# Performance work log

Measured on AMD Instinct MI355X. Metric: run time of the kernel, lower is better.

Reference implementation:

```python
import jax, jax.numpy as jnp
import numpy as np

B, T, E, H, V, O = 64, 512, 128, 256, 100000, 1


def setup_inputs() -> dict:
    key = jax.random.key(0)
    ks = jax.random.split(key, 10)
    sE, sH = 1.0 / np.sqrt(E), 1.0 / np.sqrt(H)
    return {
        "x": jax.random.randint(ks[0], (B, T), 0, V),
        "emb_table": jax.random.normal(ks[1], (V, E), jnp.float32) * 0.1,
        "W_ih": jax.random.normal(ks[2], (4 * H, E), jnp.float32) * sE,  # torch gate order i,f,g,o
        "W_hh": jax.random.normal(ks[3], (4 * H, H), jnp.float32) * sH,
        "b_ih": jnp.zeros((4 * H,), jnp.float32),  # biases init'd to 0 in source
        "b_hh": jnp.zeros((4 * H,), jnp.float32),
        "Wm": jax.random.normal(ks[4], (H, H), jnp.float32) * sH,
        "bm": jnp.zeros((H,), jnp.float32),
        "Wf": jax.random.normal(ks[5], (O, H), jnp.float32) * sH,
        "bf": jnp.zeros((O,), jnp.float32),
    }


def reference(x, emb_table, W_ih, W_hh, b_ih, b_hh, Wm, bm, Wf, bf):
    batch = x.shape[0]
    hid = W_hh.shape[1]
    # vectorized replacement for the per-(i,j) python-loop embedding copy
    embeds = emb_table[x]                                  # [B,T,E]
    # precompute input contribution to all gates for every timestep
    gx = jnp.einsum('bte,ge->btg', embeds, W_ih) + b_ih     # [B,T,4H]
    gx = jnp.swapaxes(gx, 0, 1)                             # [T,B,4H]
    h0 = jnp.zeros((batch, hid), embeds.dtype)
    c0 = jnp.zeros((batch, hid), embeds.dtype)

    def step(carry, g_t):
        h, c = carry
        g = g_t + h @ W_hh.T + b_hh                         # [B,4H]
        i, f, gg, o = jnp.split(g, 4, axis=-1)
        i, f, o = jax.nn.sigmoid(i), jax.nn.sigmoid(f), jax.nn.sigmoid(o)
        c = f * c + i * jnp.tanh(gg)
        h = o * jnp.tanh(c)
        return (h, c), h

    (hT, cT), hs = jax.lax.scan(step, (h0, c0), gx)
    out = jnp.swapaxes(hs, 0, 1)                            # [B,T,H]
    out = out @ Wm.T + bm                                   # ffmiddle
    out = out @ Wf.T + bf                                   # fc -> [B,T,O]
    sig_out = jax.nn.sigmoid(out).reshape(batch, -1).mean(axis=1)  # [B]
    # hidden = (h_n, c_n) with leading num_layers=1 dim, as in torch
    return sig_out, hT[None, :, :], cT[None, :, :]
```

## Files before the change

### kernel.cpp

```cpp
#include <hip/hip_runtime.h>


#define BATCH 64
#define TSTEPS 512
#define EDIM 128
#define HDIM 256
#define G4H 1024

typedef short bf16x8 __attribute__((ext_vector_type(8)));
typedef short bf16x4 __attribute__((ext_vector_type(4)));
typedef float f32x4 __attribute__((ext_vector_type(4)));

__device__ __forceinline__ unsigned short f2bf(float f) {
  unsigned u = __builtin_bit_cast(unsigned, f);
  return (unsigned short)((u + 0x7fffu + ((u >> 16) & 1u)) >> 16);
}
__device__ __forceinline__ float bf2f(unsigned short h) {
  unsigned u = ((unsigned)h) << 16;
  return __builtin_bit_cast(float, u);
}
__device__ __forceinline__ unsigned pk2(float a, float b) {
  return (unsigned)f2bf(a) | ((unsigned)f2bf(b) << 16);
}
__device__ __forceinline__ float fsig(float x) {
  return __builtin_amdgcn_rcpf(1.f + __expf(-x));
}
__device__ __forceinline__ float ftanh(float x) {
  return 1.f - 2.f * __builtin_amdgcn_rcpf(__expf(2.f * x) + 1.f);
}
__device__ __forceinline__ bf16x8 ldfrag(const unsigned short* p) {
  bf16x4 a = *(const bf16x4*)p;
  bf16x4 b = *(const bf16x4*)(p + 16);
  return __builtin_shufflevector(a, b, 0, 1, 2, 3, 4, 5, 6, 7);
}

__global__ __launch_bounds__(256) void k_gx(const int* __restrict__ x,
                                            const float* __restrict__ emb,
                                            const float* __restrict__ Wih,
                                            const float* __restrict__ bih,
                                            unsigned short* __restrict__ gx3) {
  const int t = blockIdx.x;
  const int g0 = blockIdx.y * 64;
  const int tid = threadIdx.x;
  __shared__ unsigned short Al[64 * 136];
  __shared__ unsigned short Bl[64 * 136];
  __shared__ int tok[64];
  if (tid < 64) tok[tid] = x[tid * TSTEPS + t];
  __syncthreads();
  {
    const int r = tid >> 2, c0 = (tid & 3) * 32;
    const float* asrc = emb + (size_t)tok[r] * EDIM + c0;
    const float* bsrc = Wih + (size_t)(g0 + r) * EDIM + c0;
#pragma unroll
    for (int s = 0; s < 32; s += 8) {
      float4 a0 = *(const float4*)(asrc + s);
      float4 a1 = *(const float4*)(asrc + s + 4);
      uint4 pa = {pk2(a0.x, a0.y), pk2(a0.z, a0.w), pk2(a1.x, a1.y), pk2(a1.z, a1.w)};
      *(uint4*)&Al[r * 136 + c0 + s] = pa;
      float4 b0 = *(const float4*)(bsrc + s);
      float4 b1 = *(const float4*)(bsrc + s + 4);
      uint4 pb = {pk2(b0.x, b0.y), pk2(b0.z, b0.w), pk2(b1.x, b1.y), pk2(b1.z, b1.w)};
      *(uint4*)&Bl[r * 136 + c0 + s] = pb;
    }
  }
  __syncthreads();
  const int lane = tid & 63, w = tid >> 6;
  const int lo = lane & 15, hi = lane >> 4;
  const int mb = (w & 1) * 32, nb = (w >> 1) * 32;
  f32x4 acc[2][2];
#pragma unroll
  for (int jj = 0; jj < 2; ++jj) {
    float bv = bih[g0 + nb + jj * 16 + lo];
    acc[0][jj] = (f32x4){bv, bv, bv, bv};
    acc[1][jj] = acc[0][jj];
  }
#pragma unroll
  for (int kk = 0; kk < 4; ++kk) {
    bf16x8 af0 = ldfrag(&Al[(mb + lo) * 136 + kk * 32 + hi * 4]);
    bf16x8 af1 = ldfrag(&Al[(mb + 16 + lo) * 136 + kk * 32 + hi * 4]);
    bf16x8 bf0 = ldfrag(&Bl[(nb + lo) * 136 + kk * 32 + hi * 4]);
    bf16x8 bf1 = ldfrag(&Bl[(nb + 16 + lo) * 136 + kk * 32 + hi * 4]);
    acc[0][0] = __builtin_amdgcn_mfma_f32_16x16x32_bf16(af0, bf0, acc[0][0], 0, 0, 0);
    acc[0][1] = __builtin_amdgcn_mfma_f32_16x16x32_bf16(af0, bf1, acc[0][1], 0, 0, 0);
    acc[1][0] = __builtin_amdgcn_mfma_f32_16x16x32_bf16(af1, bf0, acc[1][0], 0, 0, 0);
    acc[1][1] = __builtin_amdgcn_mfma_f32_16x16x32_bf16(af1, bf1, acc[1][1], 0, 0, 0);
  }
#pragma unroll
  for (int i = 0; i < 2; ++i)
#pragma unroll
    for (int jj = 0; jj < 2; ++jj)
#pragma unroll
      for (int r = 0; r < 4; ++r) {
        int m = mb + i * 16 + hi * 4 + r;
        int col = g0 + nb + jj * 16 + lo;
        int grp = m >> 4, mm = m & 15;
        int bhi = mm >> 2, br = mm & 3;
        int g = col >> 8, jc = col & 255;
        int halfb = jc >> 7, wv = (jc >> 4) & 7, lov = jc & 15;
        size_t idx = (((size_t)(t * 8 + grp * 2 + halfb) * 8 + wv) * 64 +
                      (bhi * 16 + lov)) * 16 + (g * 4 + br);
        gx3[idx] = f2bf(acc[i][jj][r]);
      }
}

__global__ __launch_bounds__(512) void k_rec(const unsigned short* __restrict__ gx3,
                                             const float* __restrict__ Whh,
                                             const float* __restrict__ bhh,
                                             unsigned long long* __restrict__ hx,
                                             unsigned short* __restrict__ hs,
                                             float* __restrict__ out) {
  const int tid = threadIdx.x;
  const int bp = blockIdx.x;
  const int grp = bp >> 1, half = bp & 1;
  const int b0 = grp * 16;
  const int lane = tid & 63, w = tid >> 6;
  const int lo = lane & 15, hi = lane >> 4;
  const int j = half * 128 + w * 16 + lo;
  __shared__ unsigned short h_lds[2][32 * 136];
  bf16x8 wf[4][8];
  float bhv[4];
#pragma unroll
  for (int g = 0; g < 4; ++g) {
    const float* wr = Whh + (size_t)(g * 256 + j) * HDIM;
    bhv[g] = bhh[g * 256 + j];
#pragma unroll
    for (int kk = 0; kk < 8; ++kk) {
      const float* p = wr + kk * 32 + hi * 8;
      float4 v0 = *(const float4*)p;
      float4 v1 = *(const float4*)(p + 4);
      bf16x8 f;
      f[0] = (short)f2bf(v0.x); f[1] = (short)f2bf(v0.y);
      f[2] = (short)f2bf(v0.z); f[3] = (short)f2bf(v0.w);
      f[4] = (short)f2bf(v1.x); f[5] = (short)f2bf(v1.y);
      f[6] = (short)f2bf(v1.z); f[7] = (short)f2bf(v1.w);
      wf[g][kk] = f;
    }
  }
  for (int i = tid; i < 32 * 136 / 2; i += 512) ((unsigned*)h_lds[0])[i] = 0u;
  const unsigned short* gp = gx3 + (((size_t)bp * 8 + w) * 64 + lane) * 16;
  unsigned gw[8];
  {
    uint4 a = *(const uint4*)(gp);
    uint4 b = *(const uint4*)(gp + 8);
    gw[0] = a.x; gw[1] = a.y; gw[2] = a.z; gw[3] = a.w;
    gw[4] = b.x; gw[5] = b.y; gw[6] = b.z; gw[7] = b.w;
  }
  float c[4] = {0.f, 0.f, 0.f, 0.f};
  const int ob = (j >> 3) * 136 + (j & 7);
  const int jp = ((half ^ 1) * 128) + ((tid >> 6) << 4) + (tid & 15);
  const int hip = (tid >> 4) & 3;
  const int pb = (jp >> 3) * 136 + (jp & 7);
  __syncthreads();
  for (int t = 0; t < TSTEPS; ++t) {
    const int cur = t & 1, nxt = cur ^ 1;
    uint4 gA, gB;
    if (t < TSTEPS - 1) {
      const unsigned short* q = gp + (size_t)(t + 1) * 65536;
      gA = *(const uint4*)(q);
      gB = *(const uint4*)(q + 8);
    }
    f32x4 acc[4];
#pragma unroll
    for (int g = 0; g < 4; ++g)
#pragma unroll
      for (int r = 0; r < 4; ++r) {
        unsigned word = gw[g * 2 + (r >> 1)];
        unsigned short v = (r & 1) ? (unsigned short)(word >> 16) : (unsigned short)word;
        acc[g][r] = bf2f(v) + bhv[g];
      }
#pragma unroll
    for (int kk = 0; kk < 8; ++kk) {
      bf16x8 a = *(const bf16x8*)&h_lds[cur][(kk * 4 + hi) * 136 + lo * 8];
      acc[0] = __builtin_amdgcn_mfma_f32_16x16x32_bf16(a, wf[0][kk], acc[0], 0, 0, 0);
      acc[1] = __builtin_amdgcn_mfma_f32_16x16x32_bf16(a, wf[1][kk], acc[1], 0, 0, 0);
      acc[2] = __builtin_amdgcn_mfma_f32_16x16x32_bf16(a, wf[2][kk], acc[2], 0, 0, 0);
      acc[3] = __builtin_amdgcn_mfma_f32_16x16x32_bf16(a, wf[3][kk], acc[3], 0, 0, 0);
    }
    gw[0] = gA.x; gw[1] = gA.y; gw[2] = gA.z; gw[3] = gA.w;
    gw[4] = gB.x; gw[5] = gB.y; gw[6] = gB.z; gw[7] = gB.w;
    float hv[4];
    unsigned short hbf[4];
#pragma unroll
    for (int r = 0; r < 4; ++r) {
      float iv = fsig(acc[0][r]);
      float fv = fsig(acc[1][r]);
      float gv = ftanh(acc[2][r]);
      float ov = fsig(acc[3][r]);
      c[r] = fv * c[r] + iv * gv;
      hv[r] = ov * ftanh(c[r]);
      hbf[r] = f2bf(hv[r]);
    }
    if (t == TSTEPS - 1) {
#pragma unroll
      for (int r = 0; r < 4; ++r) {
        const int b = b0 + hi * 4 + r;
        hs[((size_t)t * BATCH + b) * HDIM + j] = hbf[r];
        out[64 + b * HDIM + j] = hv[r];
        out[64 + BATCH * HDIM + b * HDIM + j] = c[r];
      }
      break;
    }
    const int par = (t + 1) & 1;
    const unsigned wt = (unsigned)(t + 1);
    {
      const unsigned long long tg = ((unsigned long long)wt) << 32;
      unsigned long long* dst = &hx[((size_t)(par * 8 + bp)) * 1024 + w * 128 + lane * 2];
      __hip_atomic_store(&dst[0], tg | (unsigned long long)pk2(hv[0], hv[1]),
                         __ATOMIC_RELAXED, __HIP_MEMORY_SCOPE_AGENT);
      __hip_atomic_store(&dst[1], tg | (unsigned long long)pk2(hv[2], hv[3]),
                         __ATOMIC_RELAXED, __HIP_MEMORY_SCOPE_AGENT);
    }
#pragma unroll
    for (int r = 0; r < 4; ++r) h_lds[nxt][ob + (hi * 4 + r) * 8] = hbf[r];
    {
      unsigned long long v0, v1;
      unsigned long long* src = &hx[((size_t)(par * 8 + (bp ^ 1))) * 1024 + tid * 2];
      do {
        v0 = __hip_atomic_load(&src[0], __ATOMIC_RELAXED, __HIP_MEMORY_SCOPE_AGENT);
        v1 = __hip_atomic_load(&src[1], __ATOMIC_RELAXED, __HIP_MEMORY_SCOPE_AGENT);
      } while ((unsigned)(v0 >> 32) != wt || (unsigned)(v1 >> 32) != wt);
      h_lds[nxt][pb + (hip * 4 + 0) * 8] = (unsigned short)v0;
      h_lds[nxt][pb + (hip * 4 + 1) * 8] = (unsigned short)(v0 >> 16);
      h_lds[nxt][pb + (hip * 4 + 2) * 8] = (unsigned short)v1;
      h_lds[nxt][pb + (hip * 4 + 3) * 8] = (unsigned short)(v1 >> 16);
    }
#pragma unroll
    for (int r = 0; r < 4; ++r)
      hs[((size_t)t * BATCH + (b0 + hi * 4 + r)) * HDIM + j] = hbf[r];
    __syncthreads();
  }
}

__global__ __launch_bounds__(256) void k_weff(const float* __restrict__ Wm,
                                              const float* __restrict__ bm,
                                              const float* __restrict__ Wf,
                                              const float* __restrict__ bfb,
                                              float* __restrict__ weff) {
  const int k = threadIdx.x;
  __shared__ float red[256];
  float acc = 0.f;
#pragma unroll 8
  for (int jj = 0; jj < 256; ++jj) acc += Wf[jj] * Wm[jj * 256 + k];
  weff[k] = acc;
  red[k] = bm[k] * Wf[k];
  __syncthreads();
  for (int s = 128; s > 0; s >>= 1) {
    if (k < s) red[k] += red[k + s];
    __syncthreads();
  }
  if (k == 0) weff[256] = red[0] + bfb[0];
}

__global__ __launch_bounds__(256) void k_sig(const unsigned short* __restrict__ hs,
                                             const float* __restrict__ weff,
                                             float* __restrict__ out) {
  const int b = blockIdx.x;
  const int tid = threadIdx.x, lane = tid & 63, w = tid >> 6;
  __shared__ float wlds[4];
  const float4 w4 = *(const float4*)&weff[lane * 4];
  const float c0 = weff[256];
  float acc = 0.f;
  for (int row = w; row < TSTEPS; row += 4) {
    const unsigned short* hp = &hs[((size_t)row * BATCH + b) * HDIM + lane * 4];
    ushort4 h4 = *(const ushort4*)hp;
    float s = bf2f(h4.x) * w4.x + bf2f(h4.y) * w4.y +
              bf2f(h4.z) * w4.z + bf2f(h4.w) * w4.w;
    s += __shfl_xor(s, 1);  s += __shfl_xor(s, 2);  s += __shfl_xor(s, 4);
    s += __shfl_xor(s, 8);  s += __shfl_xor(s, 16); s += __shfl_xor(s, 32);
    acc += fsig(s + c0);
  }
  if (lane == 0) wlds[w] = acc;
  __syncthreads();
  if (tid == 0) out[b] = (wlds[0] + wlds[1] + wlds[2] + wlds[3]) * (1.f / 512.f);
}

extern "C" void kernel_launch(void* const* d_in, const int* in_sizes, int n_in,
                              void* d_out, int out_size, void* d_ws, size_t ws_size,
                              hipStream_t stream) {
  (void)in_sizes; (void)n_in; (void)out_size; (void)ws_size;
  const int* x = (const int*)d_in[0];
  const float* emb = (const float*)d_in[1];
  const float* Wih = (const float*)d_in[2];
  const float* Whh = (const float*)d_in[3];
  const float* bih = (const float*)d_in[4];
  const float* bhh = (const float*)d_in[5];
  const float* Wm  = (const float*)d_in[6];
  const float* bm  = (const float*)d_in[7];
  const float* Wf  = (const float*)d_in[8];
  const float* bf  = (const float*)d_in[9];
  float* out = (float*)d_out;
  char* ws = (char*)d_ws;
  const size_t gx_bytes = (size_t)TSTEPS * BATCH * G4H * 2;
  const size_t hs_bytes = (size_t)TSTEPS * BATCH * HDIM * 2;
  const size_t hx_bytes = (size_t)2 * 8 * 1024 * 8;
  unsigned short* gx3 = (unsigned short*)ws;
  unsigned short* hs = (unsigned short*)(ws + gx_bytes);
  unsigned long long* hx = (unsigned long long*)(ws + gx_bytes + hs_bytes);
  float* weff = (float*)(ws + gx_bytes + hs_bytes + hx_bytes);
  hipMemsetAsync(hx, 0, hx_bytes, stream);
  k_gx<<<dim3(512, 16), 256, 0, stream>>>(x, emb, Wih, bih, gx3);
  k_weff<<<1, 256, 0, stream>>>(Wm, bm, Wf, bf, weff);
  k_rec<<<8, 512, 0, stream>>>(gx3, Whh, bhh, hx, hs, out);
  k_sig<<<64, 256, 0, stream>>>(hs, weff, out);
}
```

Measured before the change: 1.249 ms.

## Process two batch groups per recurrence block and fuse output head into recurrence

The recurrence kernel now runs on 4 blocks instead of 8, each handling two 16-row batch groups. The two independent MFMA chains are interleaved, so each step's latency-bound chain and cross-block handshake are amortized over twice the work. The sigmoid/mean head is computed inside the recurrence from LDS after each step, which removes the hs buffer and the separate k_sig launch. The gx store is also packed into 64-bit writes. The cost is double the per-step serial work per block (more MFMAs, activations and polls) and higher register pressure, which may lengthen the critical path.

```diff
diff --git a/kernel.cpp b/kernel.cpp
--- a/kernel.cpp
+++ b/kernel.cpp
@@ -88,35 +88,34 @@
 #pragma unroll
   for (int i = 0; i < 2; ++i)
 #pragma unroll
-    for (int jj = 0; jj < 2; ++jj)
-#pragma unroll
-      for (int r = 0; r < 4; ++r) {
-        int m = mb + i * 16 + hi * 4 + r;
-        int col = g0 + nb + jj * 16 + lo;
-        int grp = m >> 4, mm = m & 15;
-        int bhi = mm >> 2, br = mm & 3;
-        int g = col >> 8, jc = col & 255;
-        int halfb = jc >> 7, wv = (jc >> 4) & 7, lov = jc & 15;
-        size_t idx = (((size_t)(t * 8 + grp * 2 + halfb) * 8 + wv) * 64 +
-                      (bhi * 16 + lov)) * 16 + (g * 4 + br);
-        gx3[idx] = f2bf(acc[i][jj][r]);
-      }
-}
-
-__global__ __launch_bounds__(512) void k_rec(const unsigned short* __restrict__ gx3,
-                                             const float* __restrict__ Whh,
-                                             const float* __restrict__ bhh,
-                                             unsigned long long* __restrict__ hx,
-                                             unsigned short* __restrict__ hs,
-                                             float* __restrict__ out) {
+    for (int jj = 0; jj < 2; ++jj) {
+      int grp = (w & 1) * 2 + i;
+      int col = g0 + nb + jj * 16 + lo;
+      int g = col >> 8, jc = col & 255;
+      int halfb = jc >> 7, wv = (jc >> 4) & 7, lov = jc & 15;
+      size_t base = (((size_t)(t * 8 + grp * 2 + halfb) * 8 + wv) * 64 +
+                     (hi * 16 + lov)) * 16 + g * 4;
+      unsigned long long val =
+          (unsigned long long)pk2(acc[i][jj][0], acc[i][jj][1]) |
+          ((unsigned long long)pk2(acc[i][jj][2], acc[i][jj][3]) << 32);
+      *(unsigned long long*)&gx3[base] = val;
+    }
+}
+
+__global__ __launch_bounds__(512, 2) void k_rec(const unsigned short* __restrict__ gx3,
+                                                const float* __restrict__ Whh,
+                                                const float* __restrict__ bhh,
+                                                const float* __restrict__ weff,
+                                                unsigned long long* __restrict__ hx,
+                                                float* __restrict__ out) {
   const int tid = threadIdx.x;
   const int bp = blockIdx.x;
-  const int grp = bp >> 1, half = bp & 1;
-  const int b0 = grp * 16;
+  const int gpair = bp >> 1, half = bp & 1;
+  const int gA = gpair * 2, gB = gpair * 2 + 1;
   const int lane = tid & 63, w = tid >> 6;
   const int lo = lane & 15, hi = lane >> 4;
   const int j = half * 128 + w * 16 + lo;
-  __shared__ unsigned short h_lds[2][32 * 136];
+  __shared__ unsigned short h_lds[2][2][32 * 136];
   bf16x8 wf[4][8];
   float bhv[4];
 #pragma unroll
@@ -136,98 +135,170 @@
       wf[g][kk] = f;
     }
   }
-  for (int i = tid; i < 32 * 136 / 2; i += 512) ((unsigned*)h_lds[0])[i] = 0u;
-  const unsigned short* gp = gx3 + (((size_t)bp * 8 + w) * 64 + lane) * 16;
-  unsigned gw[8];
+  float wv8[8];
   {
-    uint4 a = *(const uint4*)(gp);
-    uint4 b = *(const uint4*)(gp + 8);
-    gw[0] = a.x; gw[1] = a.y; gw[2] = a.z; gw[3] = a.w;
-    gw[4] = b.x; gw[5] = b.y; gw[6] = b.z; gw[7] = b.w;
-  }
-  float c[4] = {0.f, 0.f, 0.f, 0.f};
+    const float* wp = weff + (lane & 31) * 8;
+#pragma unroll
+    for (int e = 0; e < 8; ++e) wv8[e] = wp[e];
+  }
+  const float c0 = weff[256];
+  for (int i = tid; i < 2 * 32 * 136 / 2; i += 512) {
+    ((unsigned*)h_lds[0][0])[i & (32 * 136 / 2 - 1)] = 0u;
+    ((unsigned*)h_lds[1][0])[i & (32 * 136 / 2 - 1)] = 0u;
+  }
+  const unsigned short* gpA = gx3 + (((size_t)(gA * 2 + half) * 8 + w) * 64 + lane) * 16;
+  const unsigned short* gpB = gx3 + (((size_t)(gB * 2 + half) * 8 + w) * 64 + lane) * 16;
+  unsigned gwA[8], gwB[8];
+  {
+    uint4 a = *(const uint4*)(gpA);
+    uint4 b = *(const uint4*)(gpA + 8);
+    gwA[0] = a.x; gwA[1] = a.y; gwA[2] = a.z; gwA[3] = a.w;
+    gwA[4] = b.x; gwA[5] = b.y; gwA[6] = b.z; gwA[7] = b.w;
+    uint4 c = *(const uint4*)(gpB);
+    uint4 d = *(const uint4*)(gpB + 8);
+    gwB[0] = c.x; gwB[1] = c.y; gwB[2] = c.z; gwB[3] = c.w;
+    gwB[4] = d.x; gwB[5] = d.y; gwB[6] = d.z; gwB[7] = d.w;
+  }
+  float cA[4] = {0.f, 0.f, 0.f, 0.f}, cB[4] = {0.f, 0.f, 0.f, 0.f};
+  float hvA[4], hvB[4];
+  float sig_acc = 0.f;
   const int ob = (j >> 3) * 136 + (j & 7);
   const int jp = ((half ^ 1) * 128) + ((tid >> 6) << 4) + (tid & 15);
   const int hip = (tid >> 4) & 3;
   const int pb = (jp >> 3) * 136 + (jp & 7);
+  const int sA = gA * 2 + half, sB = gB * 2 + half;
   __syncthreads();
   for (int t = 0; t < TSTEPS; ++t) {
     const int cur = t & 1, nxt = cur ^ 1;
-    uint4 gA, gB;
+    uint4 pA0, pA1, pB0, pB1;
     if (t < TSTEPS - 1) {
-      const unsigned short* q = gp + (size_t)(t + 1) * 65536;
-      gA = *(const uint4*)(q);
-      gB = *(const uint4*)(q + 8);
-    }
-    f32x4 acc[4];
+      const unsigned short* qA = gpA + (size_t)(t + 1) * 65536;
+      const unsigned short* qB = gpB + (size_t)(t + 1) * 65536;
+      pA0 = *(const uint4*)(qA);
+      pA1 = *(const uint4*)(qA + 8);
+      pB0 = *(const uint4*)(qB);
+      pB1 = *(const uint4*)(qB + 8);
+    }
+    f32x4 accA[4], accB[4];
 #pragma unroll
     for (int g = 0; g < 4; ++g)
 #pragma unroll
       for (int r = 0; r < 4; ++r) {
-        unsigned word = gw[g * 2 + (r >> 1)];
-        unsigned short v = (r & 1) ? (unsigned short)(word >> 16) : (unsigned short)word;
-        acc[g][r] = bf2f(v) + bhv[g];
+        unsigned wa = gwA[g * 2 + (r >> 1)];
+        unsigned wb = gwB[g * 2 + (r >> 1)];
+        unsigned short va = (r & 1) ? (unsigned short)(wa >> 16) : (unsigned short)wa;
+        unsigned short vb = (r & 1) ? (unsigned short)(wb >> 16) : (unsigned short)wb;
+        accA[g][r] = bf2f(va) + bhv[g];
+        accB[g][r] = bf2f(vb) + bhv[g];
       }
 #pragma unroll
     for (int kk = 0; kk < 8; ++kk) {
-      bf16x8 a = *(const bf16x8*)&h_lds[cur][(kk * 4 + hi) * 136 + lo * 8];
-      acc[0] = __builtin_amdgcn_mfma_f32_16x16x32_bf16(a, wf[0][kk], acc[0], 0, 0, 0);
-      acc[1] = __builtin_amdgcn_mfma_f32_16x16x32_bf16(a, wf[1][kk], acc[1], 0, 0, 0);
-      acc[2] = __builtin_amdgcn_mfma_f32_16x16x32_bf16(a, wf[2][kk], acc[2], 0, 0, 0);
-      acc[3] = __builtin_amdgcn_mfma_f32_16x16x32_bf16(a, wf[3][kk], acc[3], 0, 0, 0);
-    }
-    gw[0] = gA.x; gw[1] = gA.y; gw[2] = gA.z; gw[3] = gA.w;
-    gw[4] = gB.x; gw[5] = gB.y; gw[6] = gB.z; gw[7] = gB.w;
-    float hv[4];
-    unsigned short hbf[4];
+      bf16x8 a = *(const bf16x8*)&h_lds[0][cur][(kk * 4 + hi) * 136 + lo * 8];
+      accA[0] = __builtin_amdgcn_mfma_f32_16x16x32_bf16(a, wf[0][kk], accA[0], 0, 0, 0);
+      accA[1] = __builtin_amdgcn_mfma_f32_16x16x32_bf16(a, wf[1][kk], accA[1], 0, 0, 0);
+      accA[2] = __builtin_amdgcn_mfma_f32_16x16x32_bf16(a, wf[2][kk], accA[2], 0, 0, 0);
+      accA[3] = __builtin_amdgcn_mfma_f32_16x16x32_bf16(a, wf[3][kk], accA[3], 0, 0, 0);
+    }
+#pragma unroll
+    for (int kk = 0; kk < 8; ++kk) {
+      bf16x8 b = *(const bf16x8*)&h_lds[1][cur][(kk * 4 + hi) * 136 + lo * 8];
+      accB[0] = __builtin_amdgcn_mfma_f32_16x16x32_bf16(b, wf[0][kk], accB[0], 0, 0, 0);
+      accB[1] = __builtin_amdgcn_mfma_f32_16x16x32_bf16(b, wf[1][kk], accB[1], 0, 0, 0);
+      accB[2] = __builtin_amdgcn_mfma_f32_16x16x32_bf16(b, wf[2][kk], accB[2], 0, 0, 0);
+      accB[3] = __builtin_amdgcn_mfma_f32_16x16x32_bf16(b, wf[3][kk], accB[3], 0, 0, 0);
+    }
+    if (t < TSTEPS - 1) {
+      gwA[0] = pA0.x; gwA[1] = pA0.y; gwA[2] = pA0.z; gwA[3] = pA0.w;
+      gwA[4] = pA1.x; gwA[5] = pA1.y; gwA[6] = pA1.z; gwA[7] = pA1.w;
+      gwB[0] = pB0.x; gwB[1] = pB0.y; gwB[2] = pB0.z; gwB[3] = pB0.w;
+      gwB[4] = pB1.x; gwB[5] = pB1.y; gwB[6] = pB1.z; gwB[7] = pB1.w;
+    }
+    unsigned short hbA[4], hbB[4];
 #pragma unroll
     for (int r = 0; r < 4; ++r) {
-      float iv = fsig(acc[0][r]);
-      float fv = fsig(acc[1][r]);
-      float gv = ftanh(acc[2][r]);
-      float ov = fsig(acc[3][r]);
-      c[r] = fv * c[r] + iv * gv;
-      hv[r] = ov * ftanh(c[r]);
-      hbf[r] = f2bf(hv[r]);
-    }
-    if (t == TSTEPS - 1) {
-#pragma unroll
-      for (int r = 0; r < 4; ++r) {
-        const int b = b0 + hi * 4 + r;
-        hs[((size_t)t * BATCH + b) * HDIM + j] = hbf[r];
-        out[64 + b * HDIM + j] = hv[r];
-        out[64 + BATCH * HDIM + b * HDIM + j] = c[r];
-      }
-      break;
+      float iv = fsig(accA[0][r]), fv = fsig(accA[1][r]);
+      float gv = ftanh(accA[2][r]), ov = fsig(accA[3][r]);
+      cA[r] = fv * cA[r] + iv * gv;
+      hvA[r] = ov * ftanh(cA[r]);
+      hbA[r] = f2bf(hvA[r]);
+    }
+#pragma unroll
+    for (int r = 0; r < 4; ++r) {
+      float iv = fsig(accB[0][r]), fv = fsig(accB[1][r]);
+      float gv = ftanh(accB[2][r]), ov = fsig(accB[3][r]);
+      cB[r] = fv * cB[r] + iv * gv;
+      hvB[r] = ov * ftanh(cB[r]);
+      hbB[r] = f2bf(hvB[r]);
     }
     const int par = (t + 1) & 1;
     const unsigned wt = (unsigned)(t + 1);
     {
       const unsigned long long tg = ((unsigned long long)wt) << 32;
-      unsigned long long* dst = &hx[((size_t)(par * 8 + bp)) * 1024 + w * 128 + lane * 2];
-      __hip_atomic_store(&dst[0], tg | (unsigned long long)pk2(hv[0], hv[1]),
+      unsigned long long* dA = &hx[((size_t)(par * 8 + sA)) * 1024 + w * 128 + lane * 2];
+      unsigned long long* dB = &hx[((size_t)(par * 8 + sB)) * 1024 + w * 128 + lane * 2];
+      __hip_atomic_store(&dA[0], tg | (unsigned long long)pk2(hvA[0], hvA[1]),
                          __ATOMIC_RELAXED, __HIP_MEMORY_SCOPE_AGENT);
-      __hip_atomic_store(&dst[1], tg | (unsigned long long)pk2(hv[2], hv[3]),
+      __hip_atomic_store(&dA[1], tg | (unsigned long long)pk2(hvA[2], hvA[3]),
                          __ATOMIC_RELAXED, __HIP_MEMORY_SCOPE_AGENT);
-    }
-#pragma unroll
-    for (int r = 0; r < 4; ++r) h_lds[nxt][ob + (hi * 4 + r) * 8] = hbf[r];
+      __hip_atomic_store(&dB[0], tg | (unsigned long long)pk2(hvB[0], hvB[1]),
+                         __ATOMIC_RELAXED, __HIP_MEMORY_SCOPE_AGENT);
+      __hip_atomic_store(&dB[1], tg | (unsigned long long)pk2(hvB[2], hvB[3]),
+                         __ATOMIC_RELAXED, __HIP_MEMORY_SCOPE_AGENT);
+    }
+#pragma unroll
+    for (int r = 0; r < 4; ++r) {
+      h_lds[0][nxt][ob + (hi * 4 + r) * 8] = hbA[r];
+      h_lds[1][nxt][ob + (hi * 4 + r) * 8] = hbB[r];
+    }
     {
-      unsigned long long v0, v1;
-      unsigned long long* src = &hx[((size_t)(par * 8 + (bp ^ 1))) * 1024 + tid * 2];
+      unsigned long long a0, a1, b0, b1;
+      unsigned long long* qA = &hx[((size_t)(par * 8 + (sA ^ 1))) * 1024 + tid * 2];
+      unsigned long long* qB = &hx[((size_t)(par * 8 + (sB ^ 1))) * 1024 + tid * 2];
       do {
-        v0 = __hip_atomic_load(&src[0], __ATOMIC_RELAXED, __HIP_MEMORY_SCOPE_AGENT);
-        v1 = __hip_atomic_load(&src[1], __ATOMIC_RELAXED, __HIP_MEMORY_SCOPE_AGENT);
-      } while ((unsigned)(v0 >> 32) != wt || (unsigned)(v1 >> 32) != wt);
-      h_lds[nxt][pb + (hip * 4 + 0) * 8] = (unsigned short)v0;
-      h_lds[nxt][pb + (hip * 4 + 1) * 8] = (unsigned short)(v0 >> 16);
-      h_lds[nxt][pb + (hip * 4 + 2) * 8] = (unsigned short)v1;
-      h_lds[nxt][pb + (hip * 4 + 3) * 8] = (unsigned short)(v1 >> 16);
-    }
-#pragma unroll
-    for (int r = 0; r < 4; ++r)
-      hs[((size_t)t * BATCH + (b0 + hi * 4 + r)) * HDIM + j] = hbf[r];
+        a0 = __hip_atomic_load(&qA[0], __ATOMIC_RELAXED, __HIP_MEMORY_SCOPE_AGENT);
+        a1 = __hip_atomic_load(&qA[1], __ATOMIC_RELAXED, __HIP_MEMORY_SCOPE_AGENT);
+        b0 = __hip_atomic_load(&qB[0], __ATOMIC_RELAXED, __HIP_MEMORY_SCOPE_AGENT);
+        b1 = __hip_atomic_load(&qB[1], __ATOMIC_RELAXED, __HIP_MEMORY_SCOPE_AGENT);
+      } while ((unsigned)(a0 >> 32) != wt || (unsigned)(a1 >> 32) != wt ||
+               (unsigned)(b0 >> 32) != wt || (unsigned)(b1 >> 32) != wt);
+      h_lds[0][nxt][pb + (hip * 4 + 0) * 8] = (unsigned short)a0;
+      h_lds[0][nxt][pb + (hip * 4 + 1) * 8] = (unsigned short)(a0 >> 16);
+      h_lds[0][nxt][pb + (hip * 4 + 2) * 8] = (unsigned short)a1;
+      h_lds[0][nxt][pb + (hip * 4 + 3) * 8] = (unsigned short)(a1 >> 16);
+      h_lds[1][nxt][pb + (hip * 4 + 0) * 8] = (unsigned short)b0;
+      h_lds[1][nxt][pb + (hip * 4 + 1) * 8] = (unsigned short)(b0 >> 16);
+      h_lds[1][nxt][pb + (hip * 4 + 2) * 8] = (unsigned short)b1;
+      h_lds[1][nxt][pb + (hip * 4 + 3) * 8] = (unsigned short)(b1 >> 16);
+    }
     __syncthreads();
+    {
+      const int gsel = w >> 2;
+      const int bb = half * 8 + (w & 3) * 2 + (lane >> 5);
+      const int gran = lane & 31;
+      bf16x8 hv8 = *(const bf16x8*)&h_lds[gsel][nxt][gran * 136 + bb * 8];
+      float s = 0.f;
+#pragma unroll
+      for (int e = 0; e < 8; ++e) s += bf2f((unsigned short)hv8[e]) * wv8[e];
+      s += __shfl_xor(s, 1);  s += __shfl_xor(s, 2);
+      s += __shfl_xor(s, 4);  s += __shfl_xor(s, 8);
+      s += __shfl_xor(s, 16);
+      sig_acc += fsig(s + c0);
+    }
+  }
+#pragma unroll
+  for (int r = 0; r < 4; ++r) {
+    const int bA = gA * 16 + hi * 4 + r;
+    const int bB = gB * 16 + hi * 4 + r;
+    out[64 + bA * HDIM + j] = hvA[r];
+    out[64 + BATCH * HDIM + bA * HDIM + j] = cA[r];
+    out[64 + bB * HDIM + j] = hvB[r];
+    out[64 + BATCH * HDIM + bB * HDIM + j] = cB[r];
+  }
+  if ((lane & 31) == 0) {
+    const int gsel = w >> 2;
+    const int bb = half * 8 + (w & 3) * 2 + (lane >> 5);
+    const int b = (gpair * 2 + gsel) * 16 + bb;
+    out[b] = sig_acc * (1.f / 512.f);
   }
 }
 
@@ -249,29 +320,6 @@
     __syncthreads();
   }
   if (k == 0) weff[256] = red[0] + bfb[0];
-}
-
-__global__ __launch_bounds__(256) void k_sig(const unsigned short* __restrict__ hs,
-                                             const float* __restrict__ weff,
-                                             float* __restrict__ out) {
-  const int b = blockIdx.x;
-  const int tid = threadIdx.x, lane = tid & 63, w = tid >> 6;
-  __shared__ float wlds[4];
-  const float4 w4 = *(const float4*)&weff[lane * 4];
-  const float c0 = weff[256];
-  float acc = 0.f;
-  for (int row = w; row < TSTEPS; row += 4) {
-    const unsigned short* hp = &hs[((size_t)row * BATCH + b) * HDIM + lane * 4];
-    ushort4 h4 = *(const ushort4*)hp;
-    float s = bf2f(h4.x) * w4.x + bf2f(h4.y) * w4.y +
-              bf2f(h4.z) * w4.z + bf2f(h4.w) * w4.w;
-    s += __shfl_xor(s, 1);  s += __shfl_xor(s, 2);  s += __shfl_xor(s, 4);
-    s += __shfl_xor(s, 8);  s += __shfl_xor(s, 16); s += __shfl_xor(s, 32);
-    acc += fsig(s + c0);
-  }
-  if (lane == 0) wlds[w] = acc;
-  __syncthreads();
-  if (tid == 0) out[b] = (wlds[0] + wlds[1] + wlds[2] + wlds[3]) * (1.f / 512.f);
 }
 
 extern "C" void kernel_launch(void* const* d_in, const int* in_sizes, int n_in,
@@ -291,15 +339,12 @@
   float* out = (float*)d_out;
   char* ws = (char*)d_ws;
   const size_t gx_bytes = (size_t)TSTEPS * BATCH * G4H * 2;
-  const size_t hs_bytes = (size_t)TSTEPS * BATCH * HDIM * 2;
   const size_t hx_bytes = (size_t)2 * 8 * 1024 * 8;
   unsigned short* gx3 = (unsigned short*)ws;
-  unsigned short* hs = (unsigned short*)(ws + gx_bytes);
-  unsigned long long* hx = (unsigned long long*)(ws + gx_bytes + hs_bytes);
-  float* weff = (float*)(ws + gx_bytes + hs_bytes + hx_bytes);
+  unsigned long long* hx = (unsigned long long*)(ws + gx_bytes);
+  float* weff = (float*)(ws + gx_bytes + hx_bytes);
   hipMemsetAsync(hx, 0, hx_bytes, stream);
   k_gx<<<dim3(512, 16), 256, 0, stream>>>(x, emb, Wih, bih, gx3);
   k_weff<<<1, 256, 0, stream>>>(Wm, bm, Wf, bf, weff);
-  k_rec<<<8, 512, 0, stream>>>(gx3, Whh, bhh, hx, hs, out);
-  k_sig<<<64, 256, 0, stream>>>(hs, weff, out);
-}
+  k_rec<<<4, 512, 0, stream>>>(gx3, Whh, bhh, weff, hx, out);
+}
```

Result: slower. 1.860 ms (+49.0%).

## Fuse sigmoid-mean head into recurrent kernel and deepen gx prefetch

Applied to the files above, without the earlier changes.

Moves the collapsed linear head (weff dot product, sigmoid, time mean) into the recurrent kernel, so the hs buffer, its per-step global stores and the separate k_sig launch all go away. The gate-input prefetch now runs two steps ahead using two alternating register buffers, and is issued after the spin-wait instead of before the MFMAs. k_gx writes its outputs as packed 64-bit stores instead of scalar 16-bit stores. In exchange, every step of the serial loop now carries an extra LDS read, a dot product and a shuffle reduction, which lengthens the critical path of the recurrence.

```diff
diff --git a/kernel.cpp b/kernel.cpp
--- a/kernel.cpp
+++ b/kernel.cpp
@@ -32,6 +32,14 @@
   bf16x4 a = *(const bf16x4*)p;
   bf16x4 b = *(const bf16x4*)(p + 16);
   return __builtin_shufflevector(a, b, 0, 1, 2, 3, 4, 5, 6, 7);
+}
+__device__ __forceinline__ bf16x8 pack8(float4 v0, float4 v1) {
+  bf16x8 f;
+  f[0] = (short)f2bf(v0.x); f[1] = (short)f2bf(v0.y);
+  f[2] = (short)f2bf(v0.z); f[3] = (short)f2bf(v0.w);
+  f[4] = (short)f2bf(v1.x); f[5] = (short)f2bf(v1.y);
+  f[6] = (short)f2bf(v1.z); f[7] = (short)f2bf(v1.w);
+  return f;
 }
 
 __global__ __launch_bounds__(256) void k_gx(const int* __restrict__ x,
@@ -88,27 +96,26 @@
 #pragma unroll
   for (int i = 0; i < 2; ++i)
 #pragma unroll
-    for (int jj = 0; jj < 2; ++jj)
-#pragma unroll
-      for (int r = 0; r < 4; ++r) {
-        int m = mb + i * 16 + hi * 4 + r;
-        int col = g0 + nb + jj * 16 + lo;
-        int grp = m >> 4, mm = m & 15;
-        int bhi = mm >> 2, br = mm & 3;
-        int g = col >> 8, jc = col & 255;
-        int halfb = jc >> 7, wv = (jc >> 4) & 7, lov = jc & 15;
-        size_t idx = (((size_t)(t * 8 + grp * 2 + halfb) * 8 + wv) * 64 +
-                      (bhi * 16 + lov)) * 16 + (g * 4 + br);
-        gx3[idx] = f2bf(acc[i][jj][r]);
-      }
-}
-
-__global__ __launch_bounds__(512) void k_rec(const unsigned short* __restrict__ gx3,
-                                             const float* __restrict__ Whh,
-                                             const float* __restrict__ bhh,
-                                             unsigned long long* __restrict__ hx,
-                                             unsigned short* __restrict__ hs,
-                                             float* __restrict__ out) {
+    for (int jj = 0; jj < 2; ++jj) {
+      int grp = (w & 1) * 2 + i;
+      int col = g0 + nb + jj * 16 + lo;
+      int g = col >> 8, jc = col & 255;
+      int halfb = jc >> 7, wv = (jc >> 4) & 7, lov = jc & 15;
+      size_t base = (((size_t)(t * 8 + grp * 2 + halfb) * 8 + wv) * 64 +
+                     (hi * 16 + lov)) * 16 + g * 4;
+      unsigned long long val =
+          (unsigned long long)pk2(acc[i][jj][0], acc[i][jj][1]) |
+          ((unsigned long long)pk2(acc[i][jj][2], acc[i][jj][3]) << 32);
+      *(unsigned long long*)&gx3[base] = val;
+    }
+}
+
+__global__ __launch_bounds__(512, 2) void k_rec(const unsigned short* __restrict__ gx3,
+                                                const float* __restrict__ Whh,
+                                                const float* __restrict__ bhh,
+                                                const float* __restrict__ weff,
+                                                unsigned long long* __restrict__ hx,
+                                                float* __restrict__ out) {
   const int tid = threadIdx.x;
   const int bp = blockIdx.x;
   const int grp = bp >> 1, half = bp & 1;
@@ -126,45 +133,44 @@
 #pragma unroll
     for (int kk = 0; kk < 8; ++kk) {
       const float* p = wr + kk * 32 + hi * 8;
-      float4 v0 = *(const float4*)p;
-      float4 v1 = *(const float4*)(p + 4);
-      bf16x8 f;
-      f[0] = (short)f2bf(v0.x); f[1] = (short)f2bf(v0.y);
-      f[2] = (short)f2bf(v0.z); f[3] = (short)f2bf(v0.w);
-      f[4] = (short)f2bf(v1.x); f[5] = (short)f2bf(v1.y);
-      f[6] = (short)f2bf(v1.z); f[7] = (short)f2bf(v1.w);
-      wf[g][kk] = f;
-    }
-  }
+      wf[g][kk] = pack8(*(const float4*)p, *(const float4*)(p + 4));
+    }
+  }
+  const int hb_b = tid >> 5, hb_g = tid & 31;
+  float wv8[8];
+#pragma unroll
+  for (int e = 0; e < 8; ++e) wv8[e] = weff[hb_g * 8 + e];
+  const float c0 = weff[256];
+  float sig_acc = 0.f;
   for (int i = tid; i < 32 * 136 / 2; i += 512) ((unsigned*)h_lds[0])[i] = 0u;
   const unsigned short* gp = gx3 + (((size_t)bp * 8 + w) * 64 + lane) * 16;
-  unsigned gw[8];
+  unsigned gwA[8], gwB[8];
   {
     uint4 a = *(const uint4*)(gp);
     uint4 b = *(const uint4*)(gp + 8);
-    gw[0] = a.x; gw[1] = a.y; gw[2] = a.z; gw[3] = a.w;
-    gw[4] = b.x; gw[5] = b.y; gw[6] = b.z; gw[7] = b.w;
+    gwA[0] = a.x; gwA[1] = a.y; gwA[2] = a.z; gwA[3] = a.w;
+    gwA[4] = b.x; gwA[5] = b.y; gwA[6] = b.z; gwA[7] = b.w;
+    uint4 c2 = *(const uint4*)(gp + 65536);
+    uint4 d2 = *(const uint4*)(gp + 65536 + 8);
+    gwB[0] = c2.x; gwB[1] = c2.y; gwB[2] = c2.z; gwB[3] = c2.w;
+    gwB[4] = d2.x; gwB[5] = d2.y; gwB[6] = d2.z; gwB[7] = d2.w;
   }
   float c[4] = {0.f, 0.f, 0.f, 0.f};
+  float hv[4];
   const int ob = (j >> 3) * 136 + (j & 7);
   const int jp = ((half ^ 1) * 128) + ((tid >> 6) << 4) + (tid & 15);
   const int hip = (tid >> 4) & 3;
   const int pb = (jp >> 3) * 136 + (jp & 7);
   __syncthreads();
-  for (int t = 0; t < TSTEPS; ++t) {
+  auto step = [&](int t, unsigned (&G)[8]) {
     const int cur = t & 1, nxt = cur ^ 1;
-    uint4 gA, gB;
-    if (t < TSTEPS - 1) {
-      const unsigned short* q = gp + (size_t)(t + 1) * 65536;
-      gA = *(const uint4*)(q);
-      gB = *(const uint4*)(q + 8);
-    }
+    const unsigned wt = (unsigned)(t + 1);
     f32x4 acc[4];
 #pragma unroll
     for (int g = 0; g < 4; ++g)
 #pragma unroll
       for (int r = 0; r < 4; ++r) {
-        unsigned word = gw[g * 2 + (r >> 1)];
+        unsigned word = G[g * 2 + (r >> 1)];
         unsigned short v = (r & 1) ? (unsigned short)(word >> 16) : (unsigned short)word;
         acc[g][r] = bf2f(v) + bhv[g];
       }
@@ -176,32 +182,16 @@
       acc[2] = __builtin_amdgcn_mfma_f32_16x16x32_bf16(a, wf[2][kk], acc[2], 0, 0, 0);
       acc[3] = __builtin_amdgcn_mfma_f32_16x16x32_bf16(a, wf[3][kk], acc[3], 0, 0, 0);
     }
-    gw[0] = gA.x; gw[1] = gA.y; gw[2] = gA.z; gw[3] = gA.w;
-    gw[4] = gB.x; gw[5] = gB.y; gw[6] = gB.z; gw[7] = gB.w;
-    float hv[4];
     unsigned short hbf[4];
 #pragma unroll
     for (int r = 0; r < 4; ++r) {
-      float iv = fsig(acc[0][r]);
-      float fv = fsig(acc[1][r]);
-      float gv = ftanh(acc[2][r]);
-      float ov = fsig(acc[3][r]);
+      float iv = fsig(acc[0][r]), fv = fsig(acc[1][r]);
+      float gv = ftanh(acc[2][r]), ov = fsig(acc[3][r]);
       c[r] = fv * c[r] + iv * gv;
       hv[r] = ov * ftanh(c[r]);
       hbf[r] = f2bf(hv[r]);
     }
-    if (t == TSTEPS - 1) {
-#pragma unroll
-      for (int r = 0; r < 4; ++r) {
-        const int b = b0 + hi * 4 + r;
-        hs[((size_t)t * BATCH + b) * HDIM + j] = hbf[r];
-        out[64 + b * HDIM + j] = hv[r];
-        out[64 + BATCH * HDIM + b * HDIM + j] = c[r];
-      }
-      break;
-    }
-    const int par = (t + 1) & 1;
-    const unsigned wt = (unsigned)(t + 1);
+    const int par = (int)(wt & 1u);
     {
       const unsigned long long tg = ((unsigned long long)wt) << 32;
       unsigned long long* dst = &hx[((size_t)(par * 8 + bp)) * 1024 + w * 128 + lane * 2];
@@ -209,25 +199,50 @@
                          __ATOMIC_RELAXED, __HIP_MEMORY_SCOPE_AGENT);
       __hip_atomic_store(&dst[1], tg | (unsigned long long)pk2(hv[2], hv[3]),
                          __ATOMIC_RELAXED, __HIP_MEMORY_SCOPE_AGENT);
+      asm volatile("" ::: "memory");
     }
 #pragma unroll
     for (int r = 0; r < 4; ++r) h_lds[nxt][ob + (hi * 4 + r) * 8] = hbf[r];
+    unsigned long long v0, v1;
     {
-      unsigned long long v0, v1;
       unsigned long long* src = &hx[((size_t)(par * 8 + (bp ^ 1))) * 1024 + tid * 2];
       do {
         v0 = __hip_atomic_load(&src[0], __ATOMIC_RELAXED, __HIP_MEMORY_SCOPE_AGENT);
         v1 = __hip_atomic_load(&src[1], __ATOMIC_RELAXED, __HIP_MEMORY_SCOPE_AGENT);
       } while ((unsigned)(v0 >> 32) != wt || (unsigned)(v1 >> 32) != wt);
-      h_lds[nxt][pb + (hip * 4 + 0) * 8] = (unsigned short)v0;
-      h_lds[nxt][pb + (hip * 4 + 1) * 8] = (unsigned short)(v0 >> 16);
-      h_lds[nxt][pb + (hip * 4 + 2) * 8] = (unsigned short)v1;
-      h_lds[nxt][pb + (hip * 4 + 3) * 8] = (unsigned short)(v1 >> 16);
-    }
-#pragma unroll
-    for (int r = 0; r < 4; ++r)
-      hs[((size_t)t * BATCH + (b0 + hi * 4 + r)) * HDIM + j] = hbf[r];
+    }
+    if (t + 2 < TSTEPS) {
+      const unsigned short* q = gp + (size_t)(t + 2) * 65536;
+      uint4 a = *(const uint4*)(q);
+      uint4 b = *(const uint4*)(q + 8);
+      G[0] = a.x; G[1] = a.y; G[2] = a.z; G[3] = a.w;
+      G[4] = b.x; G[5] = b.y; G[6] = b.z; G[7] = b.w;
+    }
+    h_lds[nxt][pb + (hip * 4 + 0) * 8] = (unsigned short)v0;
+    h_lds[nxt][pb + (hip * 4 + 1) * 8] = (unsigned short)(v0 >> 16);
+    h_lds[nxt][pb + (hip * 4 + 2) * 8] = (unsigned short)v1;
+    h_lds[nxt][pb + (hip * 4 + 3) * 8] = (unsigned short)(v1 >> 16);
     __syncthreads();
+    {
+      bf16x8 hh = *(const bf16x8*)&h_lds[nxt][hb_g * 136 + hb_b * 8];
+      float s = 0.f;
+#pragma unroll
+      for (int e = 0; e < 8; ++e) s += bf2f((unsigned short)hh[e]) * wv8[e];
+      s += __shfl_xor(s, 1);  s += __shfl_xor(s, 2);  s += __shfl_xor(s, 4);
+      s += __shfl_xor(s, 8);  s += __shfl_xor(s, 16);
+      sig_acc += fsig(s + c0);
+    }
+  };
+  for (int t = 0; t < TSTEPS; t += 2) {
+    step(t, gwA);
+    step(t + 1, gwB);
+  }
+  if (half == 0 && hb_g == 0) out[b0 + hb_b] = sig_acc * (1.f / 512.f);
+#pragma unroll
+  for (int r = 0; r < 4; ++r) {
+    const int b = b0 + hi * 4 + r;
+    out[64 + b * HDIM + j] = hv[r];
+    out[64 + BATCH * HDIM + b * HDIM + j] = c[r];
   }
 }
 
@@ -249,29 +264,6 @@
     __syncthreads();
   }
   if (k == 0) weff[256] = red[0] + bfb[0];
-}
-
-__global__ __launch_bounds__(256) void k_sig(const unsigned short* __restrict__ hs,
-                                             const float* __restrict__ weff,
-                                             float* __restrict__ out) {
-  const int b = blockIdx.x;
-  const int tid = threadIdx.x, lane = tid & 63, w = tid >> 6;
-  __shared__ float wlds[4];
-  const float4 w4 = *(const float4*)&weff[lane * 4];
-  const float c0 = weff[256];
-  float acc = 0.f;
-  for (int row = w; row < TSTEPS; row += 4) {
-    const unsigned short* hp = &hs[((size_t)row * BATCH + b) * HDIM + lane * 4];
-    ushort4 h4 = *(const ushort4*)hp;
-    float s = bf2f(h4.x) * w4.x + bf2f(h4.y) * w4.y +
-              bf2f(h4.z) * w4.z + bf2f(h4.w) * w4.w;
-    s += __shfl_xor(s, 1);  s += __shfl_xor(s, 2);  s += __shfl_xor(s, 4);
-    s += __shfl_xor(s, 8);  s += __shfl_xor(s, 16); s += __shfl_xor(s, 32);
-    acc += fsig(s + c0);
-  }
-  if (lane == 0) wlds[w] = acc;
-  __syncthreads();
-  if (tid == 0) out[b] = (wlds[0] + wlds[1] + wlds[2] + wlds[3]) * (1.f / 512.f);
 }
 
 extern "C" void kernel_launch(void* const* d_in, const int* in_sizes, int n_in,
@@ -291,15 +283,12 @@
   float* out = (float*)d_out;
   char* ws = (char*)d_ws;
   const size_t gx_bytes = (size_t)TSTEPS * BATCH * G4H * 2;
-  const size_t hs_bytes = (size_t)TSTEPS * BATCH * HDIM * 2;
   const size_t hx_bytes = (size_t)2 * 8 * 1024 * 8;
   unsigned short* gx3 = (unsigned short*)ws;
-  unsigned short* hs = (unsigned short*)(ws + gx_bytes);
-  unsigned long long* hx = (unsigned long long*)(ws + gx_bytes + hs_bytes);
-  float* weff = (float*)(ws + gx_bytes + hs_bytes + hx_bytes);
+  unsigned long long* hx = (unsigned long long*)(ws + gx_bytes);
+  float* weff = (float*)(ws + gx_bytes + hx_bytes);
   hipMemsetAsync(hx, 0, hx_bytes, stream);
   k_gx<<<dim3(512, 16), 256, 0, stream>>>(x, emb, Wih, bih, gx3);
   k_weff<<<1, 256, 0, stream>>>(Wm, bm, Wf, bf, weff);
-  k_rec<<<8, 512, 0, stream>>>(gx3, Whh, bhh, hx, hs, out);
-  k_sig<<<64, 256, 0, stream>>>(hs, weff, out);
-}
+  k_rec<<<8, 512, 0, stream>>>(gx3, Whh, bhh, weff, hx, out);
+}
```

Result: faster. 1.197 ms (-4.1%).
